# Optimization experiments

Measured on AMD Instinct MI355X. Metric: run time of the kernel, lower is better.

Reference implementation:

```python
import jax, jax.numpy as jnp
import numpy as np

BLANK_ID = 0
B, MAX_T, MAX_U, VOCAB = 4, 200, 101, 1024  # MAX_U = max_label_len + 1


def setup_inputs() -> dict:
    key = jax.random.key(0)
    k1, k2, k3 = jax.random.split(key, 3)
    logits = jax.random.normal(k1, (B, MAX_T, MAX_U, VOCAB), dtype=jnp.float32)
    labels = jax.random.randint(k2, (B, MAX_U - 1), 0, VOCAB).astype(jnp.int64)
    label_lengths = jax.random.randint(k3, (B,), 1, MAX_U).astype(jnp.int64)  # in [1, MAX_U-1]
    attention_mask = jnp.ones((B, MAX_T), dtype=jnp.int32)
    return {"logits": logits, "labels": labels,
            "label_lengths": label_lengths, "attention_mask": attention_mask}


def _alpha_lattice(blank_lp, label_lp):
    """Forward variables for one sample.

    blank_lp: [T, U]   log P(blank | t, u)
    label_lp: [T, U-1] log P(y_u | t, u)  (label emitted at grid column u)
    Returns alpha [T, U], matching the reference recursion:
      alpha[0,0]   = blank_lp[0,0]
      alpha[t,0]   = alpha[t-1,0] + blank_lp[t,0]
      alpha[0,u]   = alpha[0,u-1] + label_lp[0,u-1]
      alpha[t,u]   = logaddexp(alpha[t-1,u]+blank_lp[t,u], alpha[t,u-1]+label_lp[t,u-1])
    """
    # First row: pure label path (cumulative sum along u).
    row0 = blank_lp[0, 0] + jnp.concatenate(
        [jnp.zeros((1,), blank_lp.dtype), jnp.cumsum(label_lp[0])])

    def time_step(prev_row, xs):
        b_t, l_t = xs                 # [U], [U-1]
        from_blank = prev_row + b_t   # blank transition into row t

        def u_step(carry, x):
            bl, lb = x
            a = jnp.logaddexp(bl, carry + lb)
            return a, a

        _, rest = jax.lax.scan(u_step, from_blank[0], (from_blank[1:], l_t))
        row = jnp.concatenate([from_blank[:1], rest])
        return row, row

    _, rows = jax.lax.scan(time_step, row0, (blank_lp[1:], label_lp[1:]))
    return jnp.concatenate([row0[None], rows], axis=0)  # [T, U]


def reference(logits, labels, label_lengths, attention_mask):
    Bn, maxT, maxU, V = logits.shape
    input_lengths = jnp.clip(attention_mask.sum(axis=1).astype(jnp.int32), 1, maxT)
    lab_lens = jnp.clip(label_lengths.astype(jnp.int32), 0, maxU - 1)
    labels_c = jnp.clip(labels, 0, V - 1)

    lp = jax.nn.log_softmax(logits, axis=-1)          # [B, T, U, V]
    blank_lp = lp[..., BLANK_ID]                      # [B, T, U]
    # label_lp[b, t, u] = lp[b, t, u, labels[b, u]] for u in [0, U-2]
    idx = jnp.broadcast_to(labels_c[:, None, :, None], (Bn, maxT, maxU - 1, 1))
    label_lp = jnp.take_along_axis(lp[:, :, :-1, :], idx, axis=3)[..., 0]

    alpha = jax.vmap(_alpha_lattice)(blank_lp, label_lp)  # [B, T, U]

    t_idx = input_lengths - 1
    u_idx = lab_lens                                  # U_b - 1 = label_len
    loss_b = -alpha[jnp.arange(Bn), t_idx, u_idx]

    valid = (input_lengths > 0) & (lab_lens > 0)
    loss_b = jnp.where(valid, loss_b, 0.0)
    num_valid = jnp.maximum(valid.sum(), 1)
    return loss_b.sum() / num_valid                   # reduction='mean'
```

## Files before the change

### kernel.cpp

```cpp
#include <hip/hip_runtime.h>
#include <math.h>

#define BB 4
#define TT 200
#define UU 101
#define VV 1024
#define NCELL (BB*TT*UU)
#define PAD 102

__device__ __forceinline__ float f4max(const float4& v) {
    return fmaxf(fmaxf(v.x, v.y), fmaxf(v.z, v.w));
}
__device__ __forceinline__ float f4comp(const float4& v, int c) {
    switch (c & 3) { case 0: return v.x; case 1: return v.y; case 2: return v.z; default: return v.w; }
}

__global__ __launch_bounds__(256) void lse_kernel(
        const float* __restrict__ logits,
        const int*   __restrict__ labels,
        const int*   __restrict__ lab_lens,
        float* __restrict__ blank_lp,
        float* __restrict__ label_lp) {
    const int wave = threadIdx.x >> 6;
    const int lane = threadIdx.x & 63;
    const int cell = blockIdx.x * 4 + wave;
    if (cell >= NCELL) return;
    const int b   = cell / (TT * UU);
    const int rem = cell % (TT * UU);
    const int t   = rem / UU;
    const int u   = rem % UU;

    int lab = lab_lens[b];
    lab = min(max(lab, 0), UU - 1);
    if (u > lab) return;

    const float4* src = (const float4*)(logits + (size_t)cell * VV);
    float4 x0 = src[lane];
    float4 x1 = src[lane + 64];
    float4 x2 = src[lane + 128];
    float4 x3 = src[lane + 192];

    float m = fmaxf(fmaxf(f4max(x0), f4max(x1)), fmaxf(f4max(x2), f4max(x3)));
    #pragma unroll
    for (int off = 32; off; off >>= 1) m = fmaxf(m, __shfl_xor(m, off));

    float s = 0.f;
    s += __expf(x0.x - m) + __expf(x0.y - m) + __expf(x0.z - m) + __expf(x0.w - m);
    s += __expf(x1.x - m) + __expf(x1.y - m) + __expf(x1.z - m) + __expf(x1.w - m);
    s += __expf(x2.x - m) + __expf(x2.y - m) + __expf(x2.z - m) + __expf(x2.w - m);
    s += __expf(x3.x - m) + __expf(x3.y - m) + __expf(x3.z - m) + __expf(x3.w - m);
    #pragma unroll
    for (int off = 32; off; off >>= 1) s += __shfl_xor(s, off);

    const float lse = m + __logf(s);

    if (lane == 0) blank_lp[cell] = x0.x - lse;

    if (u < lab) {
        int l = labels[b * (UU - 1) + u];
        l = min(max(l, 0), VV - 1);
        const int lane_l = (l >> 2) & 63;
        if (lane == lane_l) {
            const int j = l >> 8;
            const int c = l & 3;
            float val = (j == 0) ? f4comp(x0, c) : (j == 1) ? f4comp(x1, c)
                      : (j == 2) ? f4comp(x2, c) : f4comp(x3, c);
            label_lp[(b * TT + t) * (UU - 1) + u] = val - lse;
        }
    }
}

__global__ __launch_bounds__(256) void alpha_kernel(
        const float* __restrict__ blank_lp,
        const float* __restrict__ label_lp,
        const int*   __restrict__ lab_lens,
        const int*   __restrict__ attn,
        float* __restrict__ loss_b,
        int*   __restrict__ valid_b) {
    const int b    = blockIdx.x;
    const int tid  = threadIdx.x;
    const int lane = tid & 63;

    extern __shared__ float smem[];
    float* bs = smem;
    float* ls = smem + TT * PAD;

    const float* bl = blank_lp + b * TT * UU;
    const float* lb = label_lp + b * TT * (UU - 1);

    for (int i = tid; i < TT * UU; i += 256) {
        int t = i / UU, u = i - t * UU;
        bs[t * PAD + u] = bl[i];
    }
    for (int i = tid; i < TT * (UU - 1); i += 256) {
        int t = i / (UU - 1), u = i - t * (UU - 1);
        ls[t * PAD + u] = lb[i];
    }

    int acc = 0;
    for (int i = lane; i < TT; i += 64) acc += attn[b * TT + i];
    #pragma unroll
    for (int off = 32; off; off >>= 1) acc += __shfl_xor(acc, off);
    const int tmax = min(max(acc, 1), TT) - 1;
    int lab = lab_lens[b];
    lab = min(max(lab, 0), UU - 1);
    const int ndiag = tmax + lab + 1;

    __syncthreads();
    if (tid >= 64) return;

    const int uA  = lane;
    const int uB  = lane + 64;
    const int uBc = min(uB, UU - 1);
    const int eA  = max(uA - 1, 0);
    const int eB  = uBc - 1;

    auto fetch = [&](int d, float& fbA, float& flA, float& fbB, float& flB) {
        int tA = min(max(d - uA, 0), TT - 1);
        int tB = min(max(d - uB, 0), TT - 1);
        fbA = bs[tA * PAD + uA];
        flA = ls[tA * PAD + eA];
        fbB = bs[tB * PAD + uBc];
        flB = ls[tB * PAD + eB];
    };

    float aA = -INFINITY, aB = -INFINITY;

    float cbA[4], clA[4], cbB[4], clB[4];
    float nbA[4], nlA[4], nbB[4], nlB[4];
    #pragma unroll
    for (int k = 0; k < 4; ++k) fetch(k, cbA[k], clA[k], cbB[k], clB[k]);

    const int ng = (ndiag + 3) >> 2;
    for (int g = 0; g < ng; ++g) {
        const int dbase = g * 4;
        #pragma unroll
        for (int k = 0; k < 4; ++k) fetch(dbase + 4 + k, nbA[k], nlA[k], nbB[k], nlB[k]);
        #pragma unroll
        for (int k = 0; k < 4; ++k) {
            const int d = dbase + k;
            if (d < ndiag) {
                const float leftA = __shfl_up(aA, 1);
                const float upB   = __shfl_up(aB, 1);
                const float wrapB = __shfl(aA, 63);
                const float leftB = (lane == 0) ? wrapB : upB;
                const int tA = d - uA;
                const int tB = d - uB;
                {
                    const float x  = aA + cbA[k];
                    const float y  = leftA + clA[k];
                    const float mx = fmaxf(x, y), mn = fminf(x, y);
                    const float full = mx + __logf(1.f + __expf(mn - mx));
                    const float v = (d == 0) ? cbA[k]
                                  : (uA == 0) ? x
                                  : (tA == 0) ? y
                                  : full;
                    const bool act = (uA <= lab) && (tA >= 0) && (tA <= tmax);
                    aA = act ? v : aA;
                }
                {
                    const float x  = aB + cbB[k];
                    const float y  = leftB + clB[k];
                    const float mx = fmaxf(x, y), mn = fminf(x, y);
                    const float full = mx + __logf(1.f + __expf(mn - mx));
                    const float v = (tB == 0) ? y : full;
                    const bool act = (uB <= lab) && (tB >= 0) && (tB <= tmax);
                    aB = act ? v : aB;
                }
            }
        }
        #pragma unroll
        for (int k = 0; k < 4; ++k) { cbA[k] = nbA[k]; clA[k] = nlA[k];
                                      cbB[k] = nbB[k]; clB[k] = nlB[k]; }
    }

    const float cand = (lab >= 64) ? aB : aA;
    const float v = __shfl(cand, lab & 63);
    if (lane == 0) {
        loss_b[b]  = -v;
        valid_b[b] = (lab > 0) ? 1 : 0;
    }
}

__global__ void finalize_kernel(const float* __restrict__ loss_b,
                                const int* __restrict__ valid_b,
                                float* __restrict__ out) {
    if (threadIdx.x == 0 && blockIdx.x == 0) {
        float s = 0.f;
        int nv = 0;
        for (int b = 0; b < BB; ++b) {
            if (valid_b[b]) { s += loss_b[b]; ++nv; }
        }
        out[0] = s / (float)max(nv, 1);
    }
}

extern "C" void kernel_launch(void* const* d_in, const int* in_sizes, int n_in,
                              void* d_out, int out_size, void* d_ws, size_t ws_size,
                              hipStream_t stream) {
    const float* logits   = (const float*)d_in[0];
    const int*   labels   = (const int*)d_in[1];
    const int*   lab_lens = (const int*)d_in[2];
    const int*   attn     = (const int*)d_in[3];

    float* ws      = (float*)d_ws;
    float* blank   = ws;
    float* label   = blank + BB * TT * UU;
    float* loss_b  = label + BB * TT * (UU - 1);
    int*   valid_b = (int*)(loss_b + BB);

    static bool attr_set = false;
    if (!attr_set) {
        hipFuncSetAttribute((const void*)alpha_kernel,
                            hipFuncAttributeMaxDynamicSharedMemorySize,
                            2 * TT * PAD * (int)sizeof(float));
        attr_set = true;
    }

    lse_kernel<<<(NCELL + 3) / 4, 256, 0, stream>>>(logits, labels, lab_lens, blank, label);
    alpha_kernel<<<BB, 256, 2 * TT * PAD * sizeof(float), stream>>>(
        blank, label, lab_lens, attn, loss_b, valid_b);
    finalize_kernel<<<1, 64, 0, stream>>>(loss_b, valid_b, (float*)d_out);
}
```

Before: 473.7 us.

## Fuse finalize into alpha kernel, interleave lane columns, copy only active labels

Removes the separate finalize kernel launch. The last-finishing alpha block now does the mean reduction, using an atomic done-counter that lse_kernel resets to zero. The shared-memory fill now copies only the columns up to the label length, row by row per wave. Each lane now owns two adjacent u columns instead of u and u+64, so the left neighbour is an in-register value plus one shuffle rather than three shuffles. The cost is atomics and a threadfence at the end of the alpha kernel.

```diff
diff --git a/kernel.cpp b/kernel.cpp
--- a/kernel.cpp
+++ b/kernel.cpp
@@ -20,7 +20,10 @@
         const int*   __restrict__ labels,
         const int*   __restrict__ lab_lens,
         float* __restrict__ blank_lp,
-        float* __restrict__ label_lp) {
+        float* __restrict__ label_lp,
+        int*   __restrict__ done_ctr) {
+    if (blockIdx.x == 0 && threadIdx.x == 0) *done_ctr = 0;
+
     const int wave = threadIdx.x >> 6;
     const int lane = threadIdx.x & 63;
     const int cell = blockIdx.x * 4 + wave;
@@ -76,51 +79,55 @@
         const int*   __restrict__ lab_lens,
         const int*   __restrict__ attn,
         float* __restrict__ loss_b,
-        int*   __restrict__ valid_b) {
+        int*   __restrict__ valid_b,
+        int*   __restrict__ done_ctr,
+        float* __restrict__ out) {
     const int b    = blockIdx.x;
     const int tid  = threadIdx.x;
     const int lane = tid & 63;
+    const int wave = tid >> 6;
 
     extern __shared__ float smem[];
     float* bs = smem;
     float* ls = smem + TT * PAD;
 
+    int lab = lab_lens[b];
+    lab = min(max(lab, 0), UU - 1);
+
     const float* bl = blank_lp + b * TT * UU;
     const float* lb = label_lp + b * TT * (UU - 1);
 
-    for (int i = tid; i < TT * UU; i += 256) {
-        int t = i / UU, u = i - t * UU;
-        bs[t * PAD + u] = bl[i];
-    }
-    for (int i = tid; i < TT * (UU - 1); i += 256) {
-        int t = i / (UU - 1), u = i - t * (UU - 1);
-        ls[t * PAD + u] = lb[i];
-    }
+    for (int t = wave; t < TT; t += 4) {
+        const float* brow = bl + t * UU;
+        float*       bsr  = bs + t * PAD;
+        for (int u = lane; u <= lab; u += 64) bsr[u] = brow[u];
+        const float* lrow = lb + t * (UU - 1);
+        float*       lsr  = ls + t * PAD;
+        for (int u = lane; u < lab; u += 64) lsr[u] = lrow[u];
+    }
+    __syncthreads();
+    if (tid >= 64) return;
 
     int acc = 0;
     for (int i = lane; i < TT; i += 64) acc += attn[b * TT + i];
     #pragma unroll
     for (int off = 32; off; off >>= 1) acc += __shfl_xor(acc, off);
     const int tmax = min(max(acc, 1), TT) - 1;
-    int lab = lab_lens[b];
-    lab = min(max(lab, 0), UU - 1);
     const int ndiag = tmax + lab + 1;
 
-    __syncthreads();
-    if (tid >= 64) return;
-
-    const int uA  = lane;
-    const int uB  = lane + 64;
-    const int uBc = min(uB, UU - 1);
-    const int eA  = max(uA - 1, 0);
-    const int eB  = uBc - 1;
+    const int uA = lane * 2;
+    const int uB = uA + 1;
+    const int cA = min(uA, UU - 1);
+    const int cB = min(uB, UU - 1);
+    const int eA = min(max(uA - 1, 0), UU - 2);
+    const int eB = min(uB - 1, UU - 2);
 
     auto fetch = [&](int d, float& fbA, float& flA, float& fbB, float& flB) {
         int tA = min(max(d - uA, 0), TT - 1);
         int tB = min(max(d - uB, 0), TT - 1);
-        fbA = bs[tA * PAD + uA];
+        fbA = bs[tA * PAD + cA];
         flA = ls[tA * PAD + eA];
-        fbB = bs[tB * PAD + uBc];
+        fbB = bs[tB * PAD + cB];
         flB = ls[tB * PAD + eB];
     };
 
@@ -140,10 +147,8 @@
         for (int k = 0; k < 4; ++k) {
             const int d = dbase + k;
             if (d < ndiag) {
-                const float leftA = __shfl_up(aA, 1);
-                const float upB   = __shfl_up(aB, 1);
-                const float wrapB = __shfl(aA, 63);
-                const float leftB = (lane == 0) ? wrapB : upB;
+                const float leftA = __shfl_up(aB, 1);
+                const float leftB = aA;
                 const int tA = d - uA;
                 const int tB = d - uB;
                 {
@@ -174,24 +179,24 @@
                                       cbB[k] = nbB[k]; clB[k] = nlB[k]; }
     }
 
-    const float cand = (lab >= 64) ? aB : aA;
-    const float v = __shfl(cand, lab & 63);
+    const float cand = (lab & 1) ? aB : aA;
+    const float v = __shfl(cand, lab >> 1);
+
     if (lane == 0) {
-        loss_b[b]  = -v;
-        valid_b[b] = (lab > 0) ? 1 : 0;
-    }
-}
-
-__global__ void finalize_kernel(const float* __restrict__ loss_b,
-                                const int* __restrict__ valid_b,
-                                float* __restrict__ out) {
-    if (threadIdx.x == 0 && blockIdx.x == 0) {
-        float s = 0.f;
-        int nv = 0;
-        for (int b = 0; b < BB; ++b) {
-            if (valid_b[b]) { s += loss_b[b]; ++nv; }
+        atomicExch(&loss_b[b], -v);
+        atomicExch(&valid_b[b], (lab > 0) ? 1 : 0);
+        __threadfence();
+        const int prev = atomicAdd(done_ctr, 1);
+        if (prev == BB - 1) {
+            float s = 0.f; int nv = 0;
+            #pragma unroll
+            for (int i = 0; i < BB; ++i) {
+                const float li = atomicAdd(&loss_b[i], 0.0f);
+                const int   vi = atomicAdd(&valid_b[i], 0);
+                if (vi) { s += li; ++nv; }
+            }
+            out[0] = s / (float)max(nv, 1);
         }
-        out[0] = s / (float)max(nv, 1);
     }
 }
 
@@ -208,6 +213,7 @@
     float* label   = blank + BB * TT * UU;
     float* loss_b  = label + BB * TT * (UU - 1);
     int*   valid_b = (int*)(loss_b + BB);
+    int*   done    = valid_b + BB;
 
     static bool attr_set = false;
     if (!attr_set) {
@@ -217,8 +223,8 @@
         attr_set = true;
     }
 
-    lse_kernel<<<(NCELL + 3) / 4, 256, 0, stream>>>(logits, labels, lab_lens, blank, label);
+    lse_kernel<<<(NCELL + 3) / 4, 256, 0, stream>>>(logits, labels, lab_lens,
+                                                    blank, label, done);
     alpha_kernel<<<BB, 256, 2 * TT * PAD * sizeof(float), stream>>>(
-        blank, label, lab_lens, attn, loss_b, valid_b);
-    finalize_kernel<<<1, 64, 0, stream>>>(loss_b, valid_b, (float*)d_out);
-}
+        blank, label, lab_lens, attn, loss_b, valid_b, done, (float*)d_out);
+}
```

Measured after the change: 503.7 us. 6.3% more time.
